# Performance work log

Measured on AMD Instinct MI355X. Metric: run time of the kernel, lower is better.

The kernel has to match this reference:

```python
import jax, jax.numpy as jnp
import numpy as np

LATENT = 10
MAXLEN = 80
DT = 0.1
STEPS = int(round(1.0 / DT))
HIDDEN = 32
BATCH = 512


def _score_fn(xt_bld, time_b1, W1, b1, W2, b2):
    # score_model: flatten (B, L, D) -> concat time -> Dense(32, relu) -> Dense(D)
    B = xt_bld.shape[0]
    h = jnp.concatenate([xt_bld.reshape(B, -1), time_b1], axis=-1)  # (B, L*D+1)
    h = jax.nn.relu(h @ W1 + b1)
    return h @ W2 + b2  # (B, D)


def setup_inputs() -> dict:
    key = jax.random.key(0)
    k1, k2, k3, k4 = jax.random.split(key, 4)
    fan_in = MAXLEN * LATENT + 1  # 801
    z_mean = jax.random.normal(k1, (BATCH, MAXLEN, LATENT), jnp.float32)
    z_log_var = 0.1 * jax.random.normal(k2, (BATCH, MAXLEN, LATENT), jnp.float32)
    W1 = jax.random.normal(k3, (fan_in, HIDDEN), jnp.float32) / np.sqrt(fan_in)
    b1 = jnp.zeros((HIDDEN,), jnp.float32)
    W2 = jax.random.normal(k4, (HIDDEN, LATENT), jnp.float32) / np.sqrt(HIDDEN)
    b2 = jnp.zeros((LATENT,), jnp.float32)
    return {"z_mean": z_mean, "z_log_var": z_log_var, "W1": W1, "b1": b1, "W2": W2, "b2": b2}


def _diffusion_loss(z_mean, z_log_var, W1, b1, W2, b2):
    B = z_mean.shape[0]
    sigma = jnp.exp(z_log_var)                    # ez_log_var in train_step
    mu_tr = jnp.transpose(z_mean, (1, 0, 2))      # (L, B, D)
    sigma_tr = jnp.transpose(sigma, (1, 0, 2))    # (L, B, D)
    zero = jnp.zeros((1, B, LATENT), mu_tr.dtype)
    full_mu_ext = jnp.concatenate([zero, mu_tr], axis=0)       # (L+1, B, D)
    full_sigma_ext = jnp.concatenate([zero, sigma_tr], axis=0)  # (L+1, B, D)
    noise_keys = jax.random.split(jax.random.key(1337), MAXLEN * (STEPS + 1)).reshape(MAXLEN, STEPS + 1)

    def diffusion_step(i, mu_i, sigma_i, keys):
        # mask_below_target_step: keep rows < i
        mask = (jnp.arange(MAXLEN) < i).astype(mu_tr.dtype)[:, None, None]
        masked_mu = mu_tr * mask                                   # (L, B, D)
        times = i.astype(jnp.float32) + jnp.arange(STEPS, dtype=jnp.float32) * DT
        sigma_std = jnp.sqrt(sigma_i)                              # (B, D)
        x0 = mu_i + sigma_std * jax.random.normal(keys[0], (B, LATENT))

        def body(xt, xs):
            t, k = xs
            t_idx = jnp.floor(t).astype(jnp.int32)
            next_mu = jax.lax.dynamic_index_in_dim(full_mu_ext, t_idx + 1, 0, keepdims=False)
            next_sigma = jax.lax.dynamic_index_in_dim(full_sigma_ext, t_idx + 1, 0, keepdims=False)
            one_hot = jax.nn.one_hot(t_idx, MAXLEN, dtype=xt.dtype)     # (L,)
            score_in = masked_mu + one_hot[:, None, None] * xt[None]    # (L, B, D)
            score_in = jnp.transpose(score_in, (1, 0, 2))               # (B, L, D)
            time_col = jnp.full((B, 1), t, xt.dtype)
            score = _score_fn(score_in, time_col, W1, b1, W2, b2)       # (B, D)
            logdx = -(xt - next_mu) / jnp.sqrt(next_sigma)
            err = jnp.abs(logdx - score)
            dW = jax.random.normal(k, (B, LATENT)) * jnp.sqrt(DT)
            xt = xt + 0.5 * jnp.square(sigma_std) * score + sigma_std * dW
            return xt, err

        xt_final, errs = jax.lax.scan(body, x0, (times, keys[1:]))
        return xt_final, errs.sum(axis=0)  # tf.reduce_sum(error, axis=0)

    seq, err = jax.vmap(diffusion_step)(jnp.arange(MAXLEN), mu_tr, sigma_tr, noise_keys)
    sequence = jnp.transpose(seq, (1, 0, 2))       # (B, L, D)
    score_error = jnp.transpose(err, (1, 0, 2))    # (B, L, D)
    return sequence, score_error


def reference(z_mean, z_log_var, W1, b1, W2, b2):
    return _diffusion_loss(z_mean, z_log_var, W1, b1, W2, b2)
```

## Files before the change

kernel.cpp:

```cpp
#include <hip/hip_runtime.h>
#include <stdint.h>

#define LATENT 10
#define MAXLEN 80
#define STEPS  10
#define HIDDEN 32
#define BATCH  512
#define NSEG   8
#define SEGL   10

__device__ __forceinline__ void tf2x32(uint32_t k0, uint32_t k1,
                                       uint32_t x0, uint32_t x1,
                                       uint32_t& o0, uint32_t& o1) {
  uint32_t ks2 = k0 ^ k1 ^ 0x1BD11BDAu;
  uint32_t v0 = x0 + k0;
  uint32_t v1 = x1 + k1;
#define TF_R(rot) { v0 += v1; v1 = (v1 << (rot)) | (v1 >> (32 - (rot))); v1 ^= v0; }
  TF_R(13) TF_R(15) TF_R(26) TF_R(6)
  v0 += k1;  v1 += ks2 + 1u;
  TF_R(17) TF_R(29) TF_R(16) TF_R(24)
  v0 += ks2; v1 += k0 + 2u;
  TF_R(13) TF_R(15) TF_R(26) TF_R(6)
  v0 += k0;  v1 += k1 + 3u;
  TF_R(17) TF_R(29) TF_R(16) TF_R(24)
  v0 += k1;  v1 += ks2 + 4u;
  TF_R(13) TF_R(15) TF_R(26) TF_R(6)
  v0 += ks2; v1 += k0 + 5u;
#undef TF_R
  o0 = v0; o1 = v1;
}

__device__ __forceinline__ float bits_to_normal(uint32_t bits) {
  const float lo = -0.99999994f;
  float f = __uint_as_float((bits >> 9) | 0x3f800000u) - 1.0f;
  float u = fmaf(f, 2.0f, lo);
  u = fmaxf(u, lo);
  float w = -log1pf(-u * u);
  float p;
  if (w < 5.0f) {
    w -= 2.5f;
    p = 2.81022636e-08f;
    p = fmaf(p, w, 3.43273939e-07f);
    p = fmaf(p, w, -3.5233877e-06f);
    p = fmaf(p, w, -4.39150654e-06f);
    p = fmaf(p, w, 0.00021858087f);
    p = fmaf(p, w, -0.00125372503f);
    p = fmaf(p, w, -0.00417768164f);
    p = fmaf(p, w, 0.246640727f);
    p = fmaf(p, w, 1.50140941f);
  } else {
    w = sqrtf(w) - 3.0f;
    p = -0.000200214257f;
    p = fmaf(p, w, 0.000100950558f);
    p = fmaf(p, w, 0.00134934322f);
    p = fmaf(p, w, -0.00367342844f);
    p = fmaf(p, w, 0.00573950773f);
    p = fmaf(p, w, -0.0076224613f);
    p = fmaf(p, w, 0.00943887047f);
    p = fmaf(p, w, 1.00167406f);
    p = fmaf(p, w, 2.83297682f);
  }
  return 1.4142135623730951f * (p * u);
}

__global__ __launch_bounds__(256) void k_pre(
    const float* __restrict__ zmean, const float* __restrict__ W1,
    float* __restrict__ localp, float* __restrict__ segtot,
    float* __restrict__ nrm) {
  __shared__ uint32_t skk[2];
  if (blockIdx.x < 512) {
    int id = blockIdx.x * 256 + threadIdx.x;
    int s = id >> 14;
    int r = id & 16383;
    int b = r >> 5, j = r & 31;
    localp[((s * SEGL) * BATCH + b) * HIDDEN + j] = 0.0f;
    float pf0 = 0.0f, pf1 = 0.0f;
    for (int t = 1; t <= SEGL; ++t) {
      int l = s * SEGL + t - 1;
      const float2* mrow = (const float2*)(zmean + (b * MAXLEN + l) * LATENT);
      float2 m0 = mrow[0], m1 = mrow[1], m2 = mrow[2], m3 = mrow[3], m4 = mrow[4];
      const float* wl = W1 + (l * LATENT) * HIDDEN + j;
      pf0 = fmaf(m0.x, wl[0 * HIDDEN], pf0);
      pf1 = fmaf(m0.y, wl[1 * HIDDEN], pf1);
      pf0 = fmaf(m1.x, wl[2 * HIDDEN], pf0);
      pf1 = fmaf(m1.y, wl[3 * HIDDEN], pf1);
      pf0 = fmaf(m2.x, wl[4 * HIDDEN], pf0);
      pf1 = fmaf(m2.y, wl[5 * HIDDEN], pf1);
      pf0 = fmaf(m3.x, wl[6 * HIDDEN], pf0);
      pf1 = fmaf(m3.y, wl[7 * HIDDEN], pf1);
      pf0 = fmaf(m4.x, wl[8 * HIDDEN], pf0);
      pf1 = fmaf(m4.y, wl[9 * HIDDEN], pf1);
      if (t < SEGL)
        localp[((s * SEGL + t) * BATCH + b) * HIDDEN + j] = pf0 + pf1;
    }
    segtot[(s * BATCH + b) * HIDDEN + j] = pf0 + pf1;
  } else {
    int blk = blockIdx.x - 512;
    int ik  = blk / 20;
    int e   = (blk % 20) * 256 + threadIdx.x;
    if (threadIdx.x == 0) {
      uint32_t a, c;
      tf2x32(0u, 1337u, 0u, (uint32_t)ik, a, c);
      skk[0] = a; skk[1] = c;
    }
    __syncthreads();
    uint32_t o0, o1;
    tf2x32(skk[0], skk[1], 0u, (uint32_t)e, o0, o1);
    nrm[ik * 5120 + e] = bits_to_normal(o0 ^ o1);
  }
}

__global__ __launch_bounds__(256) void k_chain(
    const float* __restrict__ zmean, const float* __restrict__ zlv,
    const float* __restrict__ W1, const float* __restrict__ b1v,
    const float* __restrict__ W2, const float* __restrict__ b2v,
    const float* __restrict__ localp, const float* __restrict__ segtot,
    const float* __restrict__ nrm,
    float* __restrict__ outSeq, float* __restrict__ outErr) {
  const int tid = threadIdx.x;
  const int r = tid & 7;
  const int jb = r * 4;
  const int i = blockIdx.x >> 4;
  const int b = ((blockIdx.x & 15) << 5) + (tid >> 3);

  const float* rowT = W1 + (MAXLEN * LATENT) * HIDDEN;
  float pf[4], wT[4];
  {
    float4 l0 = *(const float4*)(localp + ((size_t)i * BATCH + b) * HIDDEN + jb);
    pf[0] = l0.x; pf[1] = l0.y; pf[2] = l0.z; pf[3] = l0.w;
    const int shi = i / SEGL;
    for (int s2 = 0; s2 < shi; ++s2) {
      float4 t0 = *(const float4*)(segtot + ((size_t)s2 * BATCH + b) * HIDDEN + jb);
      pf[0] += t0.x; pf[1] += t0.y; pf[2] += t0.z; pf[3] += t0.w;
    }
    const float fi = (float)i;
#pragma unroll
    for (int k = 0; k < 4; ++k) {
      wT[k] = rowT[jb + k];
      pf[k] = fmaf(fi, wT[k], pf[k] + b1v[jb + k]);
    }
  }

  const int base = (b * MAXLEN + i) * LATENT;
  float mu[LATENT], sstd[LATENT], u[LATENT], errs[LATENT], b2[LATENT];
  {
    const float2* zm = (const float2*)(zmean + base);
    const float2* zl = (const float2*)(zlv + base);
#pragma unroll
    for (int p = 0; p < 5; ++p) {
      float2 m = zm[p], v = zl[p];
      mu[2 * p] = m.x; mu[2 * p + 1] = m.y;
      sstd[2 * p] = sqrtf(expf(v.x));
      sstd[2 * p + 1] = sqrtf(expf(v.y));
    }
  }
#pragma unroll
  for (int d = 0; d < LATENT; ++d) { b2[d] = b2v[d]; errs[d] = 0.0f; }

  const float* nbase = nrm + (size_t)(i * (STEPS + 1)) * (BATCH * LATENT) + b * LATENT;
  {
    const float2* np = (const float2*)nbase;
#pragma unroll
    for (int p = 0; p < 5; ++p) { float2 n = np[p]; u[2 * p] = n.x; u[2 * p + 1] = n.y; }
  }

  const float* W1i = W1 + (i * LATENT) * HIDDEN + jb;
  const float* W2q = W2 + jb * LATENT;
  const float SQRT_DT = 0.31622776601683794f;

  for (int s = 0; s < STEPS; ++s) {
    float nd[LATENT];
    {
      const float2* np = (const float2*)(nbase + (s + 1) * (BATCH * LATENT));
#pragma unroll
      for (int p = 0; p < 5; ++p) { float2 n = np[p]; nd[2 * p] = n.x; nd[2 * p + 1] = n.y; }
    }
    float xt[LATENT];
#pragma unroll
    for (int d = 0; d < LATENT; ++d) xt[d] = fmaf(sstd[d], u[d], mu[d]);

    const float ts = (float)s * 0.1f;
    float h[4];
#pragma unroll
    for (int k = 0; k < 4; ++k) h[k] = fmaf(ts, wT[k], pf[k]);
#pragma unroll
    for (int d = 0; d < LATENT; ++d) {
      const float xd = xt[d];
      float4 w = *(const float4*)(W1i + d * HIDDEN);
      h[0] = fmaf(xd, w.x, h[0]); h[1] = fmaf(xd, w.y, h[1]);
      h[2] = fmaf(xd, w.z, h[2]); h[3] = fmaf(xd, w.w, h[3]);
    }
    float sc[LATENT];
#pragma unroll
    for (int d = 0; d < LATENT; ++d) sc[d] = 0.0f;
#pragma unroll
    for (int k = 0; k < 4; ++k) {
      const float hj = fmaxf(h[k], 0.0f);
      const float2* w2r = (const float2*)(W2q + k * LATENT);
#pragma unroll
      for (int p = 0; p < 5; ++p) {
        float2 w = w2r[p];
        sc[2 * p] = fmaf(hj, w.x, sc[2 * p]);
        sc[2 * p + 1] = fmaf(hj, w.y, sc[2 * p + 1]);
      }
    }
#pragma unroll
    for (int m = 1; m < 8; m <<= 1) {
#pragma unroll
      for (int d = 0; d < LATENT; ++d) sc[d] += __shfl_xor(sc[d], m);
    }
#pragma unroll
    for (int d = 0; d < LATENT; ++d) {
      float st = sc[d] + b2[d];
      errs[d] += fabsf(u[d] + st);
      float ndw = nd[d] * SQRT_DT;
      u[d] = u[d] + fmaf(0.5f * sstd[d], st, ndw);
    }
  }

#pragma unroll
  for (int d = 0; d < LATENT; ++d) {
    if ((d & 7) == r) {
      outSeq[base + d] = fmaf(sstd[d], u[d], mu[d]);
      outErr[base + d] = errs[d];
    }
  }
}

__global__ __launch_bounds__(64) void k_mono(
    const float* __restrict__ zmean, const float* __restrict__ zlv,
    const float* __restrict__ W1, const float* __restrict__ b1v,
    const float* __restrict__ W2, const float* __restrict__ b2v,
    float* __restrict__ outSeq, float* __restrict__ outErr) {
  int i = blockIdx.x >> 3;
  int b = ((blockIdx.x & 7) << 6) + threadIdx.x;
  float pref[HIDDEN];
#pragma unroll
  for (int j = 0; j < HIDDEN; ++j) pref[j] = 0.0f;
  for (int l = 0; l < i; ++l) {
    const float* mrow = zmean + (b * MAXLEN + l) * LATENT;
    const float* wrow = W1 + (l * LATENT) * HIDDEN;
#pragma unroll
    for (int d = 0; d < LATENT; ++d) {
      float m = mrow[d];
#pragma unroll
      for (int j = 0; j < HIDDEN; ++j) pref[j] = fmaf(m, wrow[d * HIDDEN + j], pref[j]);
    }
  }
  const int base = (b * MAXLEN + i) * LATENT;
  float mu[LATENT], sstd[LATENT], xt[LATENT], errs[LATENT];
#pragma unroll
  for (int d = 0; d < LATENT; ++d) {
    mu[d] = zmean[base + d];
    sstd[d] = sqrtf(expf(zlv[base + d]));
  }
  float n0[LATENT];
  {
    uint32_t a, c;
    tf2x32(0u, 1337u, 0u, (uint32_t)(i * (STEPS + 1)), a, c);
#pragma unroll
    for (int d = 0; d < LATENT; ++d) {
      uint32_t o0, o1;
      tf2x32(a, c, 0u, (uint32_t)(b * LATENT + d), o0, o1);
      n0[d] = bits_to_normal(o0 ^ o1);
    }
  }
#pragma unroll
  for (int d = 0; d < LATENT; ++d) { xt[d] = mu[d] + sstd[d] * n0[d]; errs[d] = 0.0f; }
  const float* rowT  = W1 + (MAXLEN * LATENT) * HIDDEN;
  const float* rowsI = W1 + (i * LATENT) * HIDDEN;
  const float SQRT_DT = 0.31622776601683794f;
  for (int s = 0; s < STEPS; ++s) {
    float t = (float)i + (float)s * 0.1f;
    float h[HIDDEN];
#pragma unroll
    for (int j = 0; j < HIDDEN; ++j) h[j] = pref[j];
#pragma unroll
    for (int d = 0; d < LATENT; ++d) {
      float xd = xt[d];
      const float* row = rowsI + d * HIDDEN;
#pragma unroll
      for (int j = 0; j < HIDDEN; ++j) h[j] = fmaf(xd, row[j], h[j]);
    }
    float sc[LATENT];
#pragma unroll
    for (int d = 0; d < LATENT; ++d) sc[d] = b2v[d];
#pragma unroll
    for (int j = 0; j < HIDDEN; ++j) {
      float hj = fmaf(t, rowT[j], h[j]) + b1v[j];
      hj = fmaxf(hj, 0.0f);
      const float* w2r = W2 + j * LATENT;
#pragma unroll
      for (int d = 0; d < LATENT; ++d) sc[d] = fmaf(hj, w2r[d], sc[d]);
    }
    float nd[LATENT];
    {
      uint32_t a, c;
      tf2x32(0u, 1337u, 0u, (uint32_t)(i * (STEPS + 1) + s + 1), a, c);
#pragma unroll
      for (int d = 0; d < LATENT; ++d) {
        uint32_t o0, o1;
        tf2x32(a, c, 0u, (uint32_t)(b * LATENT + d), o0, o1);
        nd[d] = bits_to_normal(o0 ^ o1);
      }
    }
#pragma unroll
    for (int d = 0; d < LATENT; ++d) {
      float logdx = -(xt[d] - mu[d]) / sstd[d];
      errs[d] += fabsf(logdx - sc[d]);
      float dW = nd[d] * SQRT_DT;
      xt[d] = xt[d] + (0.5f * (sstd[d] * sstd[d])) * sc[d] + sstd[d] * dW;
    }
  }
#pragma unroll
  for (int d = 0; d < LATENT; ++d) {
    outSeq[base + d] = xt[d];
    outErr[base + d] = errs[d];
  }
}

extern "C" void kernel_launch(void* const* d_in, const int* in_sizes, int n_in,
                              void* d_out, int out_size, void* d_ws, size_t ws_size,
                              hipStream_t stream) {
  (void)in_sizes; (void)n_in; (void)out_size;
  const float* zmean = (const float*)d_in[0];
  const float* zlv   = (const float*)d_in[1];
  const float* W1    = (const float*)d_in[2];
  const float* b1v   = (const float*)d_in[3];
  const float* W2    = (const float*)d_in[4];
  const float* b2v   = (const float*)d_in[5];
  float* outSeq = (float*)d_out;
  float* outErr = outSeq + (size_t)BATCH * MAXLEN * LATENT;

  const size_t nrmBytes   = (size_t)MAXLEN * (STEPS + 1) * BATCH * LATENT * sizeof(float);
  const size_t localBytes = (size_t)MAXLEN * BATCH * HIDDEN * sizeof(float);
  const size_t segBytes   = (size_t)NSEG * BATCH * HIDDEN * sizeof(float);

  if (ws_size >= nrmBytes + localBytes + segBytes) {
    float* nrm    = (float*)d_ws;
    float* localp = (float*)((char*)d_ws + nrmBytes);
    float* segtot = (float*)((char*)d_ws + nrmBytes + localBytes);
    hipLaunchKernelGGL(k_pre, dim3(512 + MAXLEN * (STEPS + 1) * 20), dim3(256), 0, stream,
                       zmean, W1, localp, segtot, nrm);
    hipLaunchKernelGGL(k_chain, dim3(MAXLEN * 16), dim3(256), 0, stream,
                       zmean, zlv, W1, b1v, W2, b2v, localp, segtot, nrm, outSeq, outErr);
  } else {
    hipLaunchKernelGGL(k_mono, dim3(MAXLEN * 8), dim3(64), 0, stream,
                       zmean, zlv, W1, b1v, W2, b2v, outSeq, outErr);
  }
}
```

Before: 121.5 us.

## Pad noise buffer to 16 floats per row, preload W2, reorder pre-kernel blocks

Stores the precomputed normal noise with a padded stride of 16 floats per batch row, so the chain kernel can fetch it with aligned float4 loads instead of five float2 loads. Each noise block now produces two elements per thread, and those blocks are placed before the matmul-prefix blocks in the pre-kernel grid. W2's per-thread 4x10 slice is loaded into registers once instead of being re-read every step. In exchange the noise workspace grows by 60%, and the chain kernel uses 40 more registers, which may lower occupancy.

```diff
diff --git a/kernel.cpp b/kernel.cpp
--- a/kernel.cpp
+++ b/kernel.cpp
@@ -8,6 +8,7 @@
 #define BATCH  512
 #define NSEG   8
 #define SEGL   10
+#define NPAD   16
 
 __device__ __forceinline__ void tf2x32(uint32_t k0, uint32_t k1,
                                        uint32_t x0, uint32_t x1,
@@ -68,8 +69,29 @@
     float* __restrict__ localp, float* __restrict__ segtot,
     float* __restrict__ nrm) {
   __shared__ uint32_t skk[2];
-  if (blockIdx.x < 512) {
-    int id = blockIdx.x * 256 + threadIdx.x;
+  const int tid = threadIdx.x;
+  if (blockIdx.x < 8800) {
+    int blk = blockIdx.x;
+    int ik = blk / 10;
+    int part = blk - ik * 10;
+    if (tid == 0) {
+      uint32_t a, c;
+      tf2x32(0u, 1337u, 0u, (uint32_t)ik, a, c);
+      skk[0] = a; skk[1] = c;
+    }
+    __syncthreads();
+    const uint32_t ka = skk[0], kc = skk[1];
+#pragma unroll
+    for (int h2 = 0; h2 < 2; ++h2) {
+      uint32_t e = (uint32_t)(part * 256 + tid + h2 * 2560);
+      uint32_t b = e / 10u;
+      uint32_t d = e - b * 10u;
+      uint32_t o0, o1;
+      tf2x32(ka, kc, 0u, e, o0, o1);
+      nrm[(size_t)ik * (BATCH * NPAD) + b * NPAD + d] = bits_to_normal(o0 ^ o1);
+    }
+  } else {
+    int id = (blockIdx.x - 8800) * 256 + tid;
     int s = id >> 14;
     int r = id & 16383;
     int b = r >> 5, j = r & 31;
@@ -94,19 +116,6 @@
         localp[((s * SEGL + t) * BATCH + b) * HIDDEN + j] = pf0 + pf1;
     }
     segtot[(s * BATCH + b) * HIDDEN + j] = pf0 + pf1;
-  } else {
-    int blk = blockIdx.x - 512;
-    int ik  = blk / 20;
-    int e   = (blk % 20) * 256 + threadIdx.x;
-    if (threadIdx.x == 0) {
-      uint32_t a, c;
-      tf2x32(0u, 1337u, 0u, (uint32_t)ik, a, c);
-      skk[0] = a; skk[1] = c;
-    }
-    __syncthreads();
-    uint32_t o0, o1;
-    tf2x32(skk[0], skk[1], 0u, (uint32_t)e, o0, o1);
-    nrm[ik * 5120 + e] = bits_to_normal(o0 ^ o1);
   }
 }
 
@@ -141,6 +150,16 @@
     }
   }
 
+  float w2f[40];
+  {
+    const float2* w2p = (const float2*)(W2 + jb * LATENT);
+#pragma unroll
+    for (int p = 0; p < 20; ++p) {
+      float2 w = w2p[p];
+      w2f[2 * p] = w.x; w2f[2 * p + 1] = w.y;
+    }
+  }
+
   const int base = (b * MAXLEN + i) * LATENT;
   float mu[LATENT], sstd[LATENT], u[LATENT], errs[LATENT], b2[LATENT];
   {
@@ -157,23 +176,29 @@
 #pragma unroll
   for (int d = 0; d < LATENT; ++d) { b2[d] = b2v[d]; errs[d] = 0.0f; }
 
-  const float* nbase = nrm + (size_t)(i * (STEPS + 1)) * (BATCH * LATENT) + b * LATENT;
-  {
-    const float2* np = (const float2*)nbase;
-#pragma unroll
-    for (int p = 0; p < 5; ++p) { float2 n = np[p]; u[2 * p] = n.x; u[2 * p + 1] = n.y; }
+  const float* nb = nrm + (size_t)(i * (STEPS + 1)) * (BATCH * NPAD) + b * NPAD;
+  {
+    float4 a0 = *(const float4*)nb;
+    float4 a1 = *(const float4*)(nb + 4);
+    float2 a2 = *(const float2*)(nb + 8);
+    u[0] = a0.x; u[1] = a0.y; u[2] = a0.z; u[3] = a0.w;
+    u[4] = a1.x; u[5] = a1.y; u[6] = a1.z; u[7] = a1.w;
+    u[8] = a2.x; u[9] = a2.y;
   }
 
   const float* W1i = W1 + (i * LATENT) * HIDDEN + jb;
-  const float* W2q = W2 + jb * LATENT;
   const float SQRT_DT = 0.31622776601683794f;
 
   for (int s = 0; s < STEPS; ++s) {
     float nd[LATENT];
     {
-      const float2* np = (const float2*)(nbase + (s + 1) * (BATCH * LATENT));
-#pragma unroll
-      for (int p = 0; p < 5; ++p) { float2 n = np[p]; nd[2 * p] = n.x; nd[2 * p + 1] = n.y; }
+      const float* np = nb + (size_t)(s + 1) * (BATCH * NPAD);
+      float4 a0 = *(const float4*)np;
+      float4 a1 = *(const float4*)(np + 4);
+      float2 a2 = *(const float2*)(np + 8);
+      nd[0] = a0.x; nd[1] = a0.y; nd[2] = a0.z; nd[3] = a0.w;
+      nd[4] = a1.x; nd[5] = a1.y; nd[6] = a1.z; nd[7] = a1.w;
+      nd[8] = a2.x; nd[9] = a2.y;
     }
     float xt[LATENT];
 #pragma unroll
@@ -196,13 +221,9 @@
 #pragma unroll
     for (int k = 0; k < 4; ++k) {
       const float hj = fmaxf(h[k], 0.0f);
-      const float2* w2r = (const float2*)(W2q + k * LATENT);
-#pragma unroll
-      for (int p = 0; p < 5; ++p) {
-        float2 w = w2r[p];
-        sc[2 * p] = fmaf(hj, w.x, sc[2 * p]);
-        sc[2 * p + 1] = fmaf(hj, w.y, sc[2 * p + 1]);
-      }
+#pragma unroll
+      for (int d = 0; d < LATENT; ++d)
+        sc[d] = fmaf(hj, w2f[k * LATENT + d], sc[d]);
     }
 #pragma unroll
     for (int m = 1; m < 8; m <<= 1) {
@@ -332,7 +353,7 @@
   float* outSeq = (float*)d_out;
   float* outErr = outSeq + (size_t)BATCH * MAXLEN * LATENT;
 
-  const size_t nrmBytes   = (size_t)MAXLEN * (STEPS + 1) * BATCH * LATENT * sizeof(float);
+  const size_t nrmBytes   = (size_t)MAXLEN * (STEPS + 1) * BATCH * NPAD * sizeof(float);
   const size_t localBytes = (size_t)MAXLEN * BATCH * HIDDEN * sizeof(float);
   const size_t segBytes   = (size_t)NSEG * BATCH * HIDDEN * sizeof(float);
 
@@ -340,7 +361,7 @@
     float* nrm    = (float*)d_ws;
     float* localp = (float*)((char*)d_ws + nrmBytes);
     float* segtot = (float*)((char*)d_ws + nrmBytes + localBytes);
-    hipLaunchKernelGGL(k_pre, dim3(512 + MAXLEN * (STEPS + 1) * 20), dim3(256), 0, stream,
+    hipLaunchKernelGGL(k_pre, dim3(8800 + 512), dim3(256), 0, stream,
                        zmean, W1, localp, segtot, nrm);
     hipLaunchKernelGGL(k_chain, dim3(MAXLEN * 16), dim3(256), 0, stream,
                        zmean, zlv, W1, b1v, W2, b2v, localp, segtot, nrm, outSeq, outErr);
```

After: 128.6 us. +5.9%, slower.

## Generate noise in-block into LDS and drop per-row prefix workspace

Applied to the files above, without the earlier changes.

Threefry noise generation moves from the pre-kernel into the chain kernel. Each block computes its 32x11x10 normals into shared memory, which removes the global noise buffer write and reread. The per-row prefix array (localp) is dropped. Segments shrink to 5 rows, and the chain kernel adds up segment totals plus up to 4 leftover rows directly from zmean and W1. This trades global traffic and a large pre-kernel for extra RNG and FMA work inside the chain kernel, plus some LDS use.

```diff
diff --git a/kernel.cpp b/kernel.cpp
--- a/kernel.cpp
+++ b/kernel.cpp
@@ -6,8 +6,8 @@
 #define STEPS  10
 #define HIDDEN 32
 #define BATCH  512
-#define NSEG   8
-#define SEGL   10
+#define NSEG   16
+#define SEGL   5
 
 __device__ __forceinline__ void tf2x32(uint32_t k0, uint32_t k1,
                                        uint32_t x0, uint32_t x1,
@@ -63,81 +63,98 @@
   return 1.4142135623730951f * (p * u);
 }
 
-__global__ __launch_bounds__(256) void k_pre(
+__global__ __launch_bounds__(256) void k_seg(
     const float* __restrict__ zmean, const float* __restrict__ W1,
-    float* __restrict__ localp, float* __restrict__ segtot,
-    float* __restrict__ nrm) {
-  __shared__ uint32_t skk[2];
-  if (blockIdx.x < 512) {
-    int id = blockIdx.x * 256 + threadIdx.x;
-    int s = id >> 14;
-    int r = id & 16383;
-    int b = r >> 5, j = r & 31;
-    localp[((s * SEGL) * BATCH + b) * HIDDEN + j] = 0.0f;
-    float pf0 = 0.0f, pf1 = 0.0f;
-    for (int t = 1; t <= SEGL; ++t) {
-      int l = s * SEGL + t - 1;
-      const float2* mrow = (const float2*)(zmean + (b * MAXLEN + l) * LATENT);
-      float2 m0 = mrow[0], m1 = mrow[1], m2 = mrow[2], m3 = mrow[3], m4 = mrow[4];
-      const float* wl = W1 + (l * LATENT) * HIDDEN + j;
-      pf0 = fmaf(m0.x, wl[0 * HIDDEN], pf0);
-      pf1 = fmaf(m0.y, wl[1 * HIDDEN], pf1);
-      pf0 = fmaf(m1.x, wl[2 * HIDDEN], pf0);
-      pf1 = fmaf(m1.y, wl[3 * HIDDEN], pf1);
-      pf0 = fmaf(m2.x, wl[4 * HIDDEN], pf0);
-      pf1 = fmaf(m2.y, wl[5 * HIDDEN], pf1);
-      pf0 = fmaf(m3.x, wl[6 * HIDDEN], pf0);
-      pf1 = fmaf(m3.y, wl[7 * HIDDEN], pf1);
-      pf0 = fmaf(m4.x, wl[8 * HIDDEN], pf0);
-      pf1 = fmaf(m4.y, wl[9 * HIDDEN], pf1);
-      if (t < SEGL)
-        localp[((s * SEGL + t) * BATCH + b) * HIDDEN + j] = pf0 + pf1;
-    }
-    segtot[(s * BATCH + b) * HIDDEN + j] = pf0 + pf1;
-  } else {
-    int blk = blockIdx.x - 512;
-    int ik  = blk / 20;
-    int e   = (blk % 20) * 256 + threadIdx.x;
-    if (threadIdx.x == 0) {
-      uint32_t a, c;
-      tf2x32(0u, 1337u, 0u, (uint32_t)ik, a, c);
-      skk[0] = a; skk[1] = c;
-    }
-    __syncthreads();
-    uint32_t o0, o1;
-    tf2x32(skk[0], skk[1], 0u, (uint32_t)e, o0, o1);
-    nrm[ik * 5120 + e] = bits_to_normal(o0 ^ o1);
-  }
+    float* __restrict__ segtot) {
+  int id = blockIdx.x * 256 + threadIdx.x;
+  int s = id >> 14;
+  int r = id & 16383;
+  int b = r >> 5, j = r & 31;
+  float pf0 = 0.0f, pf1 = 0.0f;
+#pragma unroll
+  for (int t = 0; t < SEGL; ++t) {
+    int l = s * SEGL + t;
+    const float2* mrow = (const float2*)(zmean + (b * MAXLEN + l) * LATENT);
+    float2 m0 = mrow[0], m1 = mrow[1], m2 = mrow[2], m3 = mrow[3], m4 = mrow[4];
+    const float* wl = W1 + (l * LATENT) * HIDDEN + j;
+    pf0 = fmaf(m0.x, wl[0 * HIDDEN], pf0);
+    pf1 = fmaf(m0.y, wl[1 * HIDDEN], pf1);
+    pf0 = fmaf(m1.x, wl[2 * HIDDEN], pf0);
+    pf1 = fmaf(m1.y, wl[3 * HIDDEN], pf1);
+    pf0 = fmaf(m2.x, wl[4 * HIDDEN], pf0);
+    pf1 = fmaf(m2.y, wl[5 * HIDDEN], pf1);
+    pf0 = fmaf(m3.x, wl[6 * HIDDEN], pf0);
+    pf1 = fmaf(m3.y, wl[7 * HIDDEN], pf1);
+    pf0 = fmaf(m4.x, wl[8 * HIDDEN], pf0);
+    pf1 = fmaf(m4.y, wl[9 * HIDDEN], pf1);
+  }
+  segtot[(s * BATCH + b) * HIDDEN + j] = pf0 + pf1;
 }
 
 __global__ __launch_bounds__(256) void k_chain(
     const float* __restrict__ zmean, const float* __restrict__ zlv,
     const float* __restrict__ W1, const float* __restrict__ b1v,
     const float* __restrict__ W2, const float* __restrict__ b2v,
-    const float* __restrict__ localp, const float* __restrict__ segtot,
-    const float* __restrict__ nrm,
+    const float* __restrict__ segtot,
     float* __restrict__ outSeq, float* __restrict__ outErr) {
+  __shared__ float nrmS[(STEPS + 1) * LATENT * 32];
+  __shared__ uint32_t skk[2 * (STEPS + 1)];
+
   const int tid = threadIdx.x;
+  const int i = blockIdx.x >> 4;
+  const int b0 = (blockIdx.x & 15) << 5;
+
+  if (tid < (STEPS + 1)) {
+    uint32_t a, c;
+    tf2x32(0u, 1337u, 0u, (uint32_t)(i * (STEPS + 1) + tid), a, c);
+    skk[2 * tid] = a; skk[2 * tid + 1] = c;
+  }
+  __syncthreads();
+
+  for (int rr = 0; rr < 14; ++rr) {
+    int idx = rr * 256 + tid;
+    if (idx < 3520) {
+      int c = idx & 31, n = idx >> 5;
+      int k = (n * 205) >> 11;
+      int d = n - k * 10;
+      uint32_t o0, o1;
+      tf2x32(skk[2 * k], skk[2 * k + 1], 0u,
+             (uint32_t)((b0 + c) * LATENT + d), o0, o1);
+      nrmS[n * 32 + c] = bits_to_normal(o0 ^ o1);
+    }
+  }
+  __syncthreads();
+
   const int r = tid & 7;
   const int jb = r * 4;
-  const int i = blockIdx.x >> 4;
-  const int b = ((blockIdx.x & 15) << 5) + (tid >> 3);
+  const int cloc = tid >> 3;
+  const int b = b0 + cloc;
 
   const float* rowT = W1 + (MAXLEN * LATENT) * HIDDEN;
   float pf[4], wT[4];
-  {
-    float4 l0 = *(const float4*)(localp + ((size_t)i * BATCH + b) * HIDDEN + jb);
-    pf[0] = l0.x; pf[1] = l0.y; pf[2] = l0.z; pf[3] = l0.w;
-    const int shi = i / SEGL;
-    for (int s2 = 0; s2 < shi; ++s2) {
-      float4 t0 = *(const float4*)(segtot + ((size_t)s2 * BATCH + b) * HIDDEN + jb);
-      pf[0] += t0.x; pf[1] += t0.y; pf[2] += t0.z; pf[3] += t0.w;
-    }
-    const float fi = (float)i;
-#pragma unroll
-    for (int k = 0; k < 4; ++k) {
-      wT[k] = rowT[jb + k];
-      pf[k] = fmaf(fi, wT[k], pf[k] + b1v[jb + k]);
+  const float fi = (float)i;
+#pragma unroll
+  for (int k = 0; k < 4; ++k) {
+    wT[k] = rowT[jb + k];
+    pf[k] = fmaf(fi, wT[k], b1v[jb + k]);
+  }
+  const int fs = i / SEGL;
+  for (int s2 = 0; s2 < fs; ++s2) {
+    float4 t0 = *(const float4*)(segtot + ((size_t)s2 * BATCH + b) * HIDDEN + jb);
+    pf[0] += t0.x; pf[1] += t0.y; pf[2] += t0.z; pf[3] += t0.w;
+  }
+  for (int l = fs * SEGL; l < i; ++l) {
+    const float2* mrow = (const float2*)(zmean + (b * MAXLEN + l) * LATENT);
+    const float* wl = W1 + (l * LATENT) * HIDDEN + jb;
+#pragma unroll
+    for (int p = 0; p < 5; ++p) {
+      float2 m = mrow[p];
+      float4 wa = *(const float4*)(wl + (2 * p) * HIDDEN);
+      float4 wb = *(const float4*)(wl + (2 * p + 1) * HIDDEN);
+      pf[0] = fmaf(m.x, wa.x, pf[0]); pf[1] = fmaf(m.x, wa.y, pf[1]);
+      pf[2] = fmaf(m.x, wa.z, pf[2]); pf[3] = fmaf(m.x, wa.w, pf[3]);
+      pf[0] = fmaf(m.y, wb.x, pf[0]); pf[1] = fmaf(m.y, wb.y, pf[1]);
+      pf[2] = fmaf(m.y, wb.z, pf[2]); pf[3] = fmaf(m.y, wb.w, pf[3]);
     }
   }
 
@@ -155,13 +172,10 @@
     }
   }
 #pragma unroll
-  for (int d = 0; d < LATENT; ++d) { b2[d] = b2v[d]; errs[d] = 0.0f; }
-
-  const float* nbase = nrm + (size_t)(i * (STEPS + 1)) * (BATCH * LATENT) + b * LATENT;
-  {
-    const float2* np = (const float2*)nbase;
-#pragma unroll
-    for (int p = 0; p < 5; ++p) { float2 n = np[p]; u[2 * p] = n.x; u[2 * p + 1] = n.y; }
+  for (int d = 0; d < LATENT; ++d) {
+    b2[d] = b2v[d];
+    errs[d] = 0.0f;
+    u[d] = nrmS[d * 32 + cloc];
   }
 
   const float* W1i = W1 + (i * LATENT) * HIDDEN + jb;
@@ -170,11 +184,10 @@
 
   for (int s = 0; s < STEPS; ++s) {
     float nd[LATENT];
-    {
-      const float2* np = (const float2*)(nbase + (s + 1) * (BATCH * LATENT));
-#pragma unroll
-      for (int p = 0; p < 5; ++p) { float2 n = np[p]; nd[2 * p] = n.x; nd[2 * p + 1] = n.y; }
-    }
+#pragma unroll
+    for (int d = 0; d < LATENT; ++d)
+      nd[d] = nrmS[((s + 1) * LATENT + d) * 32 + cloc];
+
     float xt[LATENT];
 #pragma unroll
     for (int d = 0; d < LATENT; ++d) xt[d] = fmaf(sstd[d], u[d], mu[d]);
@@ -332,18 +345,14 @@
   float* outSeq = (float*)d_out;
   float* outErr = outSeq + (size_t)BATCH * MAXLEN * LATENT;
 
-  const size_t nrmBytes   = (size_t)MAXLEN * (STEPS + 1) * BATCH * LATENT * sizeof(float);
-  const size_t localBytes = (size_t)MAXLEN * BATCH * HIDDEN * sizeof(float);
-  const size_t segBytes   = (size_t)NSEG * BATCH * HIDDEN * sizeof(float);
-
-  if (ws_size >= nrmBytes + localBytes + segBytes) {
-    float* nrm    = (float*)d_ws;
-    float* localp = (float*)((char*)d_ws + nrmBytes);
-    float* segtot = (float*)((char*)d_ws + nrmBytes + localBytes);
-    hipLaunchKernelGGL(k_pre, dim3(512 + MAXLEN * (STEPS + 1) * 20), dim3(256), 0, stream,
-                       zmean, W1, localp, segtot, nrm);
+  const size_t segBytes = (size_t)NSEG * BATCH * HIDDEN * sizeof(float);
+
+  if (ws_size >= segBytes) {
+    float* segtot = (float*)d_ws;
+    hipLaunchKernelGGL(k_seg, dim3(NSEG * BATCH * HIDDEN / 256), dim3(256), 0, stream,
+                       zmean, W1, segtot);
     hipLaunchKernelGGL(k_chain, dim3(MAXLEN * 16), dim3(256), 0, stream,
-                       zmean, zlv, W1, b1v, W2, b2v, localp, segtot, nrm, outSeq, outErr);
+                       zmean, zlv, W1, b1v, W2, b2v, segtot, outSeq, outErr);
   } else {
     hipLaunchKernelGGL(k_mono, dim3(MAXLEN * 8), dim3(64), 0, stream,
                        zmean, zlv, W1, b1v, W2, b2v, outSeq, outErr);
```

Result: slower. 124.1 us (+2.1%).
